# Performance work log

Measured on AMD Instinct MI355X. Metric: run time of the kernel, lower is better.

## Reference

```python
import jax, jax.numpy as jnp
import numpy as np

B, S, D, DFF, E, TOP_K = 4, 2048, 1024, 4096, 8, 2


def setup_inputs() -> dict:
    key = jax.random.key(0)
    ks = jax.random.split(key, 6)
    s = 0.02
    return {
        "x": jax.random.normal(ks[0], (B, S, D), dtype=jnp.float32),
        "gate_w": jax.random.normal(ks[1], (E, D), dtype=jnp.float32) * s,
        "w1": jax.random.normal(ks[2], (E, DFF, D), dtype=jnp.float32) * s,
        "b1": jax.random.normal(ks[3], (E, DFF), dtype=jnp.float32) * s,
        "w2": jax.random.normal(ks[4], (E, D, DFF), dtype=jnp.float32) * s,
        "b2": jax.random.normal(ks[5], (E, D), dtype=jnp.float32) * s,
    }


def _moe_forward(x, gate_w, w1, b1, w2, b2):
    b, s, d = x.shape
    xf = x.reshape(-1, d)                      # [T, D]
    T = xf.shape[0]
    e = gate_w.shape[0]
    logits = xf @ gate_w.T                     # [T, E]
    top_v, top_i = jax.lax.top_k(logits, TOP_K)  # [T, K]
    gw = jax.nn.softmax(top_v, axis=-1)          # [T, K]
    # load-balance loss (Switch Transformers): E * sum_i f_i * P_i
    probs = jax.nn.softmax(logits, axis=-1)
    f = jnp.mean(jax.nn.one_hot(jnp.argmax(logits, axis=-1), e, dtype=x.dtype), axis=0)
    lb_loss = e * jnp.sum(f * probs.mean(axis=0))
    # dense per-expert FFN (exact GELU, matching torch F.gelu default)
    h = jax.nn.gelu(jnp.einsum('td,efd->tef', xf, w1) + b1, approximate=False)  # [T,E,DFF]
    eo = jnp.einsum('tef,edf->ted', h, w2) + b2                                  # [T,E,D]
    # scatter top-k gate weights into dense [T, E] combine weights
    cw = jnp.zeros((T, e), dtype=x.dtype).at[jnp.arange(T)[:, None], top_i].add(gw)
    out = jnp.einsum('te,ted->td', cw, eo).reshape(b, s, d)
    return out, lb_loss


def reference(x, gate_w, w1, b1, w2, b2):
    return _moe_forward(x, gate_w, w1, b1, w2, b2)
```

## Files before the change

kernel.cpp:

```cpp
#include <hip/hip_runtime.h>
#include <cstdint>
#include <cstddef>

#define NEXP 8
#define NTOK 8192
#define DMODEL 1024
#define DFFN 4096
#define CAP 17408
#define MTILES (CAP / 128)

typedef __bf16 bf16;
typedef bf16 bf16x8 __attribute__((ext_vector_type(8)));
typedef float f32x4 __attribute__((ext_vector_type(4)));

static constexpr size_t OFF_HDR  = 0;
static constexpr size_t OFF_CNTH = 4096;
static constexpr size_t OFF_AMH  = OFF_CNTH + 65536;
static constexpr size_t OFF_PSH  = OFF_AMH + 65536;
static constexpr size_t OFF_TOKE = OFF_PSH + 65536;
static constexpr size_t OFF_TOKG = OFF_TOKE + 65536;
static constexpr size_t OFF_TOKS = OFF_TOKG + 65536;
static constexpr size_t OFF_BB   = OFF_TOKS + 65536;
static constexpr size_t OFF_XG   = OFF_BB + 65536;
static constexpr size_t OFF_W1B  = OFF_XG  + (size_t)CAP * DMODEL * 2;
static constexpr size_t OFF_W2B  = OFF_W1B + (size_t)NEXP * DFFN * DMODEL * 2;
static constexpr size_t OFF_H    = OFF_W2B + (size_t)NEXP * DMODEL * DFFN * 2;
static constexpr size_t OFF_O    = OFF_H   + (size_t)CAP * DFFN * 2;


__global__ void k_zero16(uint4* __restrict__ p) {
    p[(size_t)blockIdx.x * 256 + threadIdx.x] = make_uint4(0u, 0u, 0u, 0u);
}

__global__ void k_cvt(const float* __restrict__ s, bf16* __restrict__ d, int n8) {
    int i = blockIdx.x * 256 + threadIdx.x;
    if (i >= n8) return;
    const float4* sp = (const float4*)s;
    float4 a = sp[2 * i], b = sp[2 * i + 1];
    bf16x8 pk;
    pk[0] = (bf16)a.x; pk[1] = (bf16)a.y; pk[2] = (bf16)a.z; pk[3] = (bf16)a.w;
    pk[4] = (bf16)b.x; pk[5] = (bf16)b.y; pk[6] = (bf16)b.z; pk[7] = (bf16)b.w;
    ((bf16x8*)d)[i] = pk;
}

__global__ void k_gate(const float* __restrict__ x, const float* __restrict__ gwt,
                       int* __restrict__ cnth, int* __restrict__ amh, float* __restrict__ psh,
                       int* __restrict__ toke, float* __restrict__ tokg) {
    int tid = threadIdx.x, w = tid >> 6, lane = tid & 63;
    int t = blockIdx.x * 4 + w;
    __shared__ int s_cnt[8]; __shared__ int s_am[8]; __shared__ float s_ps[8];
    if (tid < 8) { s_cnt[tid] = 0; s_am[tid] = 0; s_ps[tid] = 0.f; }
    __syncthreads();
    float acc[8] = {0.f,0.f,0.f,0.f,0.f,0.f,0.f,0.f};
    const float4* xr = (const float4*)(x + (size_t)t * DMODEL);
#pragma unroll
    for (int c = 0; c < 4; c++) {
        float4 xv = xr[c * 64 + lane];
#pragma unroll
        for (int e = 0; e < 8; e++) {
            float4 wv = ((const float4*)(gwt + e * DMODEL))[c * 64 + lane];
            acc[e] = fmaf(xv.x, wv.x, fmaf(xv.y, wv.y, fmaf(xv.z, wv.z, fmaf(xv.w, wv.w, acc[e]))));
        }
    }
#pragma unroll
    for (int o = 32; o; o >>= 1) {
#pragma unroll
        for (int e = 0; e < 8; e++) acc[e] += __shfl_xor(acc[e], o);
    }
    if (lane == 0) {
        int i0 = 0; float v0 = acc[0];
#pragma unroll
        for (int e = 1; e < 8; e++) if (acc[e] > v0) { v0 = acc[e]; i0 = e; }
        int i1 = -1; float v1 = -1e30f;
#pragma unroll
        for (int e = 0; e < 8; e++) if (e != i0 && acc[e] > v1) { v1 = acc[e]; i1 = e; }
        float ex = expf(v1 - v0);
        float g0 = 1.f / (1.f + ex);
        float g1 = ex / (1.f + ex);
        toke[2 * t] = i0; toke[2 * t + 1] = i1;
        tokg[2 * t] = g0; tokg[2 * t + 1] = g1;
        atomicAdd(&s_cnt[i0], 1); atomicAdd(&s_cnt[i1], 1); atomicAdd(&s_am[i0], 1);
        float p[8], sum = 0.f;
#pragma unroll
        for (int e = 0; e < 8; e++) { p[e] = expf(acc[e] - v0); sum += p[e]; }
        float inv = 1.f / sum;
#pragma unroll
        for (int e = 0; e < 8; e++) atomicAdd(&s_ps[e], p[e] * inv);
    }
    __syncthreads();
    if (tid < 8) {
        cnth[blockIdx.x * 8 + tid] = s_cnt[tid];
        amh[blockIdx.x * 8 + tid]  = s_am[tid];
        psh[blockIdx.x * 8 + tid]  = s_ps[tid];
    }
}

__global__ void k_offsets(const int* __restrict__ cnth, const int* __restrict__ amh,
                          const float* __restrict__ psh, int* __restrict__ hdr,
                          int* __restrict__ bb, float* __restrict__ lb_out) {
    __shared__ int sc[8][256];
    __shared__ int sa[8][256];
    __shared__ float sp[8][256];
    __shared__ int sOff[8];
    int tid = threadIdx.x;
    int tc[8] = {0,0,0,0,0,0,0,0}, la[8] = {0,0,0,0,0,0,0,0};
    float lp[8] = {0.f,0.f,0.f,0.f,0.f,0.f,0.f,0.f};
    for (int j = 0; j < 8; j++) {
        int b = tid * 8 + j;
#pragma unroll
        for (int e = 0; e < 8; e++) { tc[e] += cnth[b * 8 + e]; la[e] += amh[b * 8 + e]; lp[e] += psh[b * 8 + e]; }
    }
#pragma unroll
    for (int e = 0; e < 8; e++) { sc[e][tid] = tc[e]; sa[e][tid] = la[e]; sp[e][tid] = lp[e]; }
    __syncthreads();
    for (int s = 1; s < 256; s <<= 1) {
        int add[8];
#pragma unroll
        for (int e = 0; e < 8; e++) add[e] = (tid >= s) ? sc[e][tid - s] : 0;
        __syncthreads();
#pragma unroll
        for (int e = 0; e < 8; e++) sc[e][tid] += add[e];
        __syncthreads();
    }
    for (int s = 128; s > 0; s >>= 1) {
        if (tid < s) {
#pragma unroll
            for (int e = 0; e < 8; e++) { sa[e][tid] += sa[e][tid + s]; sp[e][tid] += sp[e][tid + s]; }
        }
        __syncthreads();
    }
    if (tid == 0) {
        int run = 0; float lb = 0.f;
        for (int e = 0; e < 8; e++) {
            int c = sc[e][255];
            hdr[e] = c;
            hdr[16 + e] = run;
            int pad = ((c + 127) >> 7) << 7;
            hdr[24 + e] = pad;
            sOff[e] = run;
            run += pad;
            lb += ((float)sa[e][0] / (float)NTOK) * (sp[e][0] / (float)NTOK);
        }
        lb_out[0] = 8.f * lb;
    }
    __syncthreads();
    int excl[8];
#pragma unroll
    for (int e = 0; e < 8; e++) excl[e] = sOff[e] + sc[e][tid] - tc[e];
    for (int j = 0; j < 8; j++) {
        int b = tid * 8 + j;
#pragma unroll
        for (int e = 0; e < 8; e++) {
            bb[b * 8 + e] = excl[e];
            excl[e] += cnth[b * 8 + e];
        }
    }
}

__global__ void k_scatter(const float* __restrict__ x, const int* __restrict__ bb,
                          const int* __restrict__ toke, int* __restrict__ toks,
                          bf16* __restrict__ Xg) {
    int tid = threadIdx.x, w = tid >> 6, lane = tid & 63;
    int t = blockIdx.x * 4 + w;
    int a_e = (lane < 8) ? toke[blockIdx.x * 8 + lane] : 0;
    int e0 = __shfl(a_e, 2 * w), e1 = __shfl(a_e, 2 * w + 1);
    int r0 = 0, r1 = 0;
    for (int j = 0; j < 2 * w; j++) {
        int ej = __shfl(a_e, j);
        r0 += (ej == e0);
        r1 += (ej == e1);
    }
    int s0 = bb[blockIdx.x * 8 + e0] + r0;
    int s1 = bb[blockIdx.x * 8 + e1] + r1;
    if (lane == 0) { toks[2 * t] = s0; toks[2 * t + 1] = s1; }
    const float4* xr = (const float4*)(x + (size_t)t * DMODEL);
    bf16* d0 = Xg + (size_t)s0 * DMODEL;
    bf16* d1 = Xg + (size_t)s1 * DMODEL;
#pragma unroll
    for (int c = 0; c < 2; c++) {
        int base = c * 512 + lane * 8;
        float4 u = xr[base >> 2], v = xr[(base >> 2) + 1];
        bf16x8 pk;
        pk[0] = (bf16)u.x; pk[1] = (bf16)u.y; pk[2] = (bf16)u.z; pk[3] = (bf16)u.w;
        pk[4] = (bf16)v.x; pk[5] = (bf16)v.y; pk[6] = (bf16)v.z; pk[7] = (bf16)v.w;
        *(bf16x8*)(d0 + base) = pk;
        *(bf16x8*)(d1 + base) = pk;
    }
}

__device__ __forceinline__ void gll16(const bf16* g, bf16* l) {
    __builtin_amdgcn_global_load_lds((const __attribute__((address_space(1))) unsigned int*)g,
                                     (__attribute__((address_space(3))) unsigned int*)l, 16, 0, 0);
}

__device__ __forceinline__ float gelu_fast(float x) {
    float x3 = x * x * x;
    float z = fmaf(0.0713548163f, x3, 1.5957691216f * x);
    float s = __builtin_amdgcn_rcpf(1.0f + __expf(-z));
    return x * s;
}

template <int KD, int ND, bool GELU_BF16>
__global__ __launch_bounds__(256) void k_gemm(
    const bf16* __restrict__ Abase, const bf16* __restrict__ Wbase,
    const float* __restrict__ bias, void* __restrict__ Cbase,
    const int* __restrict__ hdr) {
    int flat = blockIdx.x;
    int g = flat % MTILES;
    int n = flat / MTILES;
    int row0 = g * 128;
    int total = hdr[16 + 7] + hdr[24 + 7];
    if (row0 >= total) return;
    int e = 0;
#pragma unroll
    for (int k = 1; k < 8; k++) e += (row0 >= hdr[16 + k]) ? 1 : 0;
    int nt = n * 128;

    const bf16* A = Abase + (size_t)row0 * KD;
    const bf16* W = Wbase + (size_t)e * ND * KD + (size_t)nt * KD;

    __shared__ bf16 As[128 * 64];
    __shared__ bf16 Bs[128 * 64];

    int tid = threadIdx.x, w = tid >> 6, lane = tid & 63;
    int lrow = lane >> 3;
    int lcolswz = ((lane & 7) ^ lrow) * 8;
    int wm = (w & 1) * 64, wn = (w >> 1) * 64;
    int fr = lane & 15, quad = lane >> 4;
    int swz = quad ^ (fr & 7);

    f32x4 acc[4][4] = {};

    for (int k0 = 0; k0 < KD; k0 += 64) {
#pragma unroll
        for (int i = 0; i < 4; i++) {
            int rb = w * 32 + i * 8;
            gll16(A + (size_t)(rb + lrow) * KD + k0 + lcolswz, &As[rb * 64]);
            gll16(W + (size_t)(rb + lrow) * KD + k0 + lcolswz, &Bs[rb * 64]);
        }
        __syncthreads();
#pragma unroll
        for (int kk = 0; kk < 64; kk += 32) {
            int coff = (swz ^ (kk >> 3)) * 8;
            bf16x8 af[4], bfr[4];
#pragma unroll
            for (int i = 0; i < 4; i++) af[i]  = *(const bf16x8*)&As[(wm + i * 16 + fr) * 64 + coff];
#pragma unroll
            for (int j = 0; j < 4; j++) bfr[j] = *(const bf16x8*)&Bs[(wn + j * 16 + fr) * 64 + coff];
#pragma unroll
            for (int i = 0; i < 4; i++)
#pragma unroll
                for (int j = 0; j < 4; j++)
                    acc[i][j] = __builtin_amdgcn_mfma_f32_16x16x32_bf16(af[i], bfr[j], acc[i][j], 0, 0, 0);
        }
        __syncthreads();
    }

#pragma unroll
    for (int j = 0; j < 4; j++) {
        int col = nt + wn + j * 16 + fr;
        float bv = bias[e * ND + col];
#pragma unroll
        for (int i = 0; i < 4; i++) {
#pragma unroll
            for (int r = 0; r < 4; r++) {
                int row = row0 + wm + i * 16 + quad * 4 + r;
                float v = acc[i][j][r] + bv;
                if (GELU_BF16) {
                    v = gelu_fast(v);
                    ((bf16*)Cbase)[(size_t)row * ND + col] = (bf16)v;
                } else {
                    ((float*)Cbase)[(size_t)row * ND + col] = v;
                }
            }
        }
    }
}

__global__ void k_combine(const float* __restrict__ O, const int* __restrict__ toks,
                          const float* __restrict__ tokg, float* __restrict__ out) {
    int t = blockIdx.x;
    int s0 = toks[2 * t], s1 = toks[2 * t + 1];
    float g0 = tokg[2 * t], g1 = tokg[2 * t + 1];
    const float4* o0 = (const float4*)(O + (size_t)s0 * DMODEL);
    const float4* o1 = (const float4*)(O + (size_t)s1 * DMODEL);
    float4* dst = (float4*)(out + (size_t)t * DMODEL);
    int i = threadIdx.x;
    float4 a = o0[i], b = o1[i];
    float4 r;
    r.x = g0 * a.x + g1 * b.x;
    r.y = g0 * a.y + g1 * b.y;
    r.z = g0 * a.z + g1 * b.z;
    r.w = g0 * a.w + g1 * b.w;
    dst[i] = r;
}

extern "C" void kernel_launch(void* const* d_in, const int* in_sizes, int n_in,
                              void* d_out, int out_size, void* d_ws, size_t ws_size,
                              hipStream_t stream) {
    const float* x   = (const float*)d_in[0];
    const float* gwt = (const float*)d_in[1];
    const float* w1  = (const float*)d_in[2];
    const float* b1  = (const float*)d_in[3];
    const float* w2  = (const float*)d_in[4];
    const float* b2  = (const float*)d_in[5];
    float* out = (float*)d_out;

    char* ws = (char*)d_ws;
    int*   hdr  = (int*)(ws + OFF_HDR);
    int*   cnth = (int*)(ws + OFF_CNTH);
    int*   amh  = (int*)(ws + OFF_AMH);
    float* psh  = (float*)(ws + OFF_PSH);
    int*   toke = (int*)(ws + OFF_TOKE);
    float* tokg = (float*)(ws + OFF_TOKG);
    int*   toks = (int*)(ws + OFF_TOKS);
    int*   bb   = (int*)(ws + OFF_BB);
    bf16*  Xg   = (bf16*)(ws + OFF_XG);
    bf16*  w1b  = (bf16*)(ws + OFF_W1B);
    bf16*  w2b  = (bf16*)(ws + OFF_W2B);
    bf16*  H    = (bf16*)(ws + OFF_H);
    float* O    = (float*)(ws + OFF_O);

    k_zero16<<<8704, 256, 0, stream>>>((uint4*)(ws + OFF_XG));
    k_cvt<<<16384, 256, 0, stream>>>(w1, w1b, 4194304);
    k_cvt<<<16384, 256, 0, stream>>>(w2, w2b, 4194304);
    k_gate<<<2048, 256, 0, stream>>>(x, gwt, cnth, amh, psh, toke, tokg);
    k_offsets<<<1, 256, 0, stream>>>(cnth, amh, psh, hdr, bb, out + (size_t)NTOK * DMODEL);
    k_scatter<<<2048, 256, 0, stream>>>(x, bb, toke, toks, Xg);
    k_gemm<DMODEL, DFFN, true><<<MTILES * (DFFN / 128), 256, 0, stream>>>(Xg, w1b, b1, (void*)H, hdr);
    k_gemm<DFFN, DMODEL, false><<<MTILES * (DMODEL / 128), 256, 0, stream>>>(H, w2b, b2, (void*)O, hdr);
    k_combine<<<NTOK, 256, 0, stream>>>(O, toks, tokg, out);
}
```

Before: 909.3 us.

## Pre-pack operands into MFMA fragment-major layout and drop LDS staging in GEMMs

Weights, gathered activations and the hidden tensor H are now stored in a fragment-major layout, where each 16-row by 32-k block is laid out exactly as the 16x16x32 MFMA expects. This lets the GEMM load operands straight from global memory into registers with double buffering, with no LDS tiles or block barriers in the main loop. Scatter is split into an index-only pass that builds an inverse map and a gather kernel that fills padding rows with zeros, so the separate zero-fill of Xg goes away. The trade-off is that blocks no longer share data through LDS, so global and L2 traffic rises. The first GEMM epilogue also needs an LDS transpose to write H in the packed layout.

New measurement: 1.050 ms. +15.5%, slower.

```diff
diff --git a/kernel.cpp b/kernel.cpp
--- a/kernel.cpp
+++ b/kernel.cpp
@@ -12,6 +12,7 @@
 typedef __bf16 bf16;
 typedef bf16 bf16x8 __attribute__((ext_vector_type(8)));
 typedef float f32x4 __attribute__((ext_vector_type(4)));
+
 
 static constexpr size_t OFF_HDR  = 0;
 static constexpr size_t OFF_CNTH = 4096;
@@ -21,26 +22,41 @@
 static constexpr size_t OFF_TOKG = OFF_TOKE + 65536;
 static constexpr size_t OFF_TOKS = OFF_TOKG + 65536;
 static constexpr size_t OFF_BB   = OFF_TOKS + 65536;
-static constexpr size_t OFF_XG   = OFF_BB + 65536;
+static constexpr size_t OFF_INV  = OFF_BB + 65536;
+static constexpr size_t OFF_XG   = OFF_INV + 73728;
 static constexpr size_t OFF_W1B  = OFF_XG  + (size_t)CAP * DMODEL * 2;
 static constexpr size_t OFF_W2B  = OFF_W1B + (size_t)NEXP * DFFN * DMODEL * 2;
 static constexpr size_t OFF_H    = OFF_W2B + (size_t)NEXP * DMODEL * DFFN * 2;
 static constexpr size_t OFF_O    = OFF_H   + (size_t)CAP * DFFN * 2;
 
 
-__global__ void k_zero16(uint4* __restrict__ p) {
-    p[(size_t)blockIdx.x * 256 + threadIdx.x] = make_uint4(0u, 0u, 0u, 0u);
-}
-
-__global__ void k_cvt(const float* __restrict__ s, bf16* __restrict__ d, int n8) {
-    int i = blockIdx.x * 256 + threadIdx.x;
-    if (i >= n8) return;
-    const float4* sp = (const float4*)s;
-    float4 a = sp[2 * i], b = sp[2 * i + 1];
-    bf16x8 pk;
-    pk[0] = (bf16)a.x; pk[1] = (bf16)a.y; pk[2] = (bf16)a.z; pk[3] = (bf16)a.w;
-    pk[4] = (bf16)b.x; pk[5] = (bf16)b.y; pk[6] = (bf16)b.z; pk[7] = (bf16)b.w;
-    ((bf16x8*)d)[i] = pk;
+__global__ void k_fillm1(int4* __restrict__ p) {
+    p[blockIdx.x * 256 + threadIdx.x] = make_int4(-1, -1, -1, -1);
+}
+
+template <int K>
+__global__ void k_cvt_fm(const float* __restrict__ w, bf16* __restrict__ wfm) {
+    constexpr int CB = K / 128;
+    __shared__ float ld[16][136];
+    int t = threadIdx.x;
+    int row = t >> 4, seg = t & 15;
+    int kbl = t >> 6, lane = t & 63, quad = lane >> 4, fr = lane & 15;
+    const float* src = w + (size_t)(blockIdx.x * 16 + row) * K + seg * 8;
+    bf16* dstg = wfm + (size_t)blockIdx.x * 16 * K + lane * 8;
+    for (int cb = 0; cb < CB; cb++) {
+        const float4* s = (const float4*)(src + cb * 128);
+        float4 u = s[0], v = s[1];
+        *(float4*)&ld[row][seg * 8] = u;
+        *(float4*)&ld[row][seg * 8 + 4] = v;
+        __syncthreads();
+        float4 a = *(const float4*)&ld[fr][kbl * 32 + quad * 8];
+        float4 b = *(const float4*)&ld[fr][kbl * 32 + quad * 8 + 4];
+        bf16x8 pk;
+        pk[0] = (bf16)a.x; pk[1] = (bf16)a.y; pk[2] = (bf16)a.z; pk[3] = (bf16)a.w;
+        pk[4] = (bf16)b.x; pk[5] = (bf16)b.y; pk[6] = (bf16)b.z; pk[7] = (bf16)b.w;
+        *(bf16x8*)(dstg + (size_t)(cb * 4 + kbl) * 512) = pk;
+        __syncthreads();
+    }
 }
 
 __global__ void k_gate(const float* __restrict__ x, const float* __restrict__ gwt,
@@ -157,40 +173,43 @@
     }
 }
 
-__global__ void k_scatter(const float* __restrict__ x, const int* __restrict__ bb,
-                          const int* __restrict__ toke, int* __restrict__ toks,
-                          bf16* __restrict__ Xg) {
+__global__ void k_scatter(const int* __restrict__ bb, const int* __restrict__ toke,
+                          int* __restrict__ toks, int* __restrict__ inv) {
+    int t = blockIdx.x * 256 + threadIdx.x;
+    int gb = t >> 2, k4 = t & 3;
+    int a[8];
+#pragma unroll
+    for (int j = 0; j < 8; j++) a[j] = toke[gb * 8 + j];
+    int e0 = a[2 * k4], e1 = a[2 * k4 + 1];
+    int r0 = 0, r1 = 0;
+    for (int j = 0; j < 2 * k4; j++) { r0 += (a[j] == e0); r1 += (a[j] == e1); }
+    int s0 = bb[gb * 8 + e0] + r0;
+    int s1 = bb[gb * 8 + e1] + r1;
+    toks[2 * t] = s0; toks[2 * t + 1] = s1;
+    inv[s0] = t; inv[s1] = t;
+}
+
+__global__ void k_gather(const float* __restrict__ x, const int* __restrict__ inv,
+                         bf16* __restrict__ Xg) {
+    int m16 = blockIdx.x;
     int tid = threadIdx.x, w = tid >> 6, lane = tid & 63;
-    int t = blockIdx.x * 4 + w;
-    int a_e = (lane < 8) ? toke[blockIdx.x * 8 + lane] : 0;
-    int e0 = __shfl(a_e, 2 * w), e1 = __shfl(a_e, 2 * w + 1);
-    int r0 = 0, r1 = 0;
-    for (int j = 0; j < 2 * w; j++) {
-        int ej = __shfl(a_e, j);
-        r0 += (ej == e0);
-        r1 += (ej == e1);
-    }
-    int s0 = bb[blockIdx.x * 8 + e0] + r0;
-    int s1 = bb[blockIdx.x * 8 + e1] + r1;
-    if (lane == 0) { toks[2 * t] = s0; toks[2 * t + 1] = s1; }
-    const float4* xr = (const float4*)(x + (size_t)t * DMODEL);
-    bf16* d0 = Xg + (size_t)s0 * DMODEL;
-    bf16* d1 = Xg + (size_t)s1 * DMODEL;
-#pragma unroll
-    for (int c = 0; c < 2; c++) {
-        int base = c * 512 + lane * 8;
-        float4 u = xr[base >> 2], v = xr[(base >> 2) + 1];
+    int quad = lane >> 4, fr = lane & 15;
+    int t16 = (lane < 16) ? inv[m16 * 16 + lane] : -1;
+    int tok = __shfl(t16, fr);
+    bf16* dst = Xg + (size_t)m16 * 32 * 512 + lane * 8;
+    for (int kb = w * 8; kb < w * 8 + 8; kb++) {
         bf16x8 pk;
-        pk[0] = (bf16)u.x; pk[1] = (bf16)u.y; pk[2] = (bf16)u.z; pk[3] = (bf16)u.w;
-        pk[4] = (bf16)v.x; pk[5] = (bf16)v.y; pk[6] = (bf16)v.z; pk[7] = (bf16)v.w;
-        *(bf16x8*)(d0 + base) = pk;
-        *(bf16x8*)(d1 + base) = pk;
-    }
-}
-
-__device__ __forceinline__ void gll16(const bf16* g, bf16* l) {
-    __builtin_amdgcn_global_load_lds((const __attribute__((address_space(1))) unsigned int*)g,
-                                     (__attribute__((address_space(3))) unsigned int*)l, 16, 0, 0);
+        if (tok >= 0) {
+            const float4* s = (const float4*)(x + (size_t)tok * DMODEL + kb * 32 + quad * 8);
+            float4 u = s[0], v = s[1];
+            pk[0] = (bf16)u.x; pk[1] = (bf16)u.y; pk[2] = (bf16)u.z; pk[3] = (bf16)u.w;
+            pk[4] = (bf16)v.x; pk[5] = (bf16)v.y; pk[6] = (bf16)v.z; pk[7] = (bf16)v.w;
+        } else {
+#pragma unroll
+            for (int j = 0; j < 8; j++) pk[j] = (bf16)0.f;
+        }
+        *(bf16x8*)(dst + (size_t)kb * 512) = pk;
+    }
 }
 
 __device__ __forceinline__ float gelu_fast(float x) {
@@ -202,9 +221,10 @@
 
 template <int KD, int ND, bool GELU_BF16>
 __global__ __launch_bounds__(256) void k_gemm(
-    const bf16* __restrict__ Abase, const bf16* __restrict__ Wbase,
+    const bf16* __restrict__ Afm, const bf16* __restrict__ Wfm,
     const float* __restrict__ bias, void* __restrict__ Cbase,
     const int* __restrict__ hdr) {
+    constexpr int KB = KD / 32;
     int flat = blockIdx.x;
     int g = flat % MTILES;
     int n = flat / MTILES;
@@ -216,61 +236,89 @@
     for (int k = 1; k < 8; k++) e += (row0 >= hdr[16 + k]) ? 1 : 0;
     int nt = n * 128;
 
-    const bf16* A = Abase + (size_t)row0 * KD;
-    const bf16* W = Wbase + (size_t)e * ND * KD + (size_t)nt * KD;
-
-    __shared__ bf16 As[128 * 64];
-    __shared__ bf16 Bs[128 * 64];
-
     int tid = threadIdx.x, w = tid >> 6, lane = tid & 63;
-    int lrow = lane >> 3;
-    int lcolswz = ((lane & 7) ^ lrow) * 8;
     int wm = (w & 1) * 64, wn = (w >> 1) * 64;
     int fr = lane & 15, quad = lane >> 4;
-    int swz = quad ^ (fr & 7);
+
+    const bf16* pA[4];
+    const bf16* pB[4];
+#pragma unroll
+    for (int i = 0; i < 4; i++) {
+        int m16 = ((row0 + wm) >> 4) + i;
+        pA[i] = Afm + (size_t)m16 * KB * 512 + lane * 8;
+        int n16 = ((nt + wn) >> 4) + i;
+        pB[i] = Wfm + (size_t)e * ND * KD + (size_t)n16 * KB * 512 + lane * 8;
+    }
 
     f32x4 acc[4][4] = {};
-
-    for (int k0 = 0; k0 < KD; k0 += 64) {
+    bf16x8 a0[4], b0[4], a1[4], b1[4];
+#pragma unroll
+    for (int i = 0; i < 4; i++) { a0[i] = *(const bf16x8*)(pA[i]); b0[i] = *(const bf16x8*)(pB[i]); }
+
+    for (int kb = 0; kb < KB; kb += 2) {
 #pragma unroll
         for (int i = 0; i < 4; i++) {
-            int rb = w * 32 + i * 8;
-            gll16(A + (size_t)(rb + lrow) * KD + k0 + lcolswz, &As[rb * 64]);
-            gll16(W + (size_t)(rb + lrow) * KD + k0 + lcolswz, &Bs[rb * 64]);
-        }
-        __syncthreads();
-#pragma unroll
-        for (int kk = 0; kk < 64; kk += 32) {
-            int coff = (swz ^ (kk >> 3)) * 8;
-            bf16x8 af[4], bfr[4];
-#pragma unroll
-            for (int i = 0; i < 4; i++) af[i]  = *(const bf16x8*)&As[(wm + i * 16 + fr) * 64 + coff];
-#pragma unroll
-            for (int j = 0; j < 4; j++) bfr[j] = *(const bf16x8*)&Bs[(wn + j * 16 + fr) * 64 + coff];
-#pragma unroll
-            for (int i = 0; i < 4; i++)
-#pragma unroll
-                for (int j = 0; j < 4; j++)
-                    acc[i][j] = __builtin_amdgcn_mfma_f32_16x16x32_bf16(af[i], bfr[j], acc[i][j], 0, 0, 0);
-        }
-        __syncthreads();
-    }
-
-#pragma unroll
-    for (int j = 0; j < 4; j++) {
-        int col = nt + wn + j * 16 + fr;
-        float bv = bias[e * ND + col];
-#pragma unroll
-        for (int i = 0; i < 4; i++) {
-#pragma unroll
-            for (int r = 0; r < 4; r++) {
-                int row = row0 + wm + i * 16 + quad * 4 + r;
-                float v = acc[i][j][r] + bv;
-                if (GELU_BF16) {
-                    v = gelu_fast(v);
-                    ((bf16*)Cbase)[(size_t)row * ND + col] = (bf16)v;
-                } else {
-                    ((float*)Cbase)[(size_t)row * ND + col] = v;
+            a1[i] = *(const bf16x8*)(pA[i] + (size_t)(kb + 1) * 512);
+            b1[i] = *(const bf16x8*)(pB[i] + (size_t)(kb + 1) * 512);
+        }
+#pragma unroll
+        for (int i = 0; i < 4; i++)
+#pragma unroll
+            for (int j = 0; j < 4; j++)
+                acc[i][j] = __builtin_amdgcn_mfma_f32_16x16x32_bf16(a0[i], b0[j], acc[i][j], 0, 0, 0);
+        if (kb + 2 < KB) {
+#pragma unroll
+            for (int i = 0; i < 4; i++) {
+                a0[i] = *(const bf16x8*)(pA[i] + (size_t)(kb + 2) * 512);
+                b0[i] = *(const bf16x8*)(pB[i] + (size_t)(kb + 2) * 512);
+            }
+        }
+#pragma unroll
+        for (int i = 0; i < 4; i++)
+#pragma unroll
+            for (int j = 0; j < 4; j++)
+                acc[i][j] = __builtin_amdgcn_mfma_f32_16x16x32_bf16(a1[i], b1[j], acc[i][j], 0, 0, 0);
+    }
+
+    if constexpr (GELU_BF16) {
+        __shared__ bf16 Ct[128 * 136];
+#pragma unroll
+        for (int j = 0; j < 4; j++) {
+            int lc = wn + j * 16 + fr;
+            float bv = bias[e * ND + nt + lc];
+#pragma unroll
+            for (int i = 0; i < 4; i++) {
+#pragma unroll
+                for (int r = 0; r < 4; r++) {
+                    int lr = wm + i * 16 + quad * 4 + r;
+                    Ct[lr * 136 + lc] = (bf16)gelu_fast(acc[i][j][r] + bv);
+                }
+            }
+        }
+        __syncthreads();
+        bf16* Hfm = (bf16*)Cbase;
+        constexpr int KBH = ND / 32;
+#pragma unroll
+        for (int li = 0; li < 8; li++) {
+            int line = w * 8 + li;
+            int mg = line >> 2, kbl = line & 3;
+            bf16x8 v = *(const bf16x8*)&Ct[(mg * 16 + fr) * 136 + kbl * 32 + quad * 8];
+            size_t m16 = (size_t)(row0 >> 4) + mg;
+            size_t kbG = (size_t)(nt >> 5) + kbl;
+            *(bf16x8*)(Hfm + (m16 * KBH + kbG) * 512 + lane * 8) = v;
+        }
+    } else {
+        float* Ob = (float*)Cbase;
+#pragma unroll
+        for (int j = 0; j < 4; j++) {
+            int col = nt + wn + j * 16 + fr;
+            float bv = bias[e * ND + col];
+#pragma unroll
+            for (int i = 0; i < 4; i++) {
+#pragma unroll
+                for (int r = 0; r < 4; r++) {
+                    int row = row0 + wm + i * 16 + quad * 4 + r;
+                    Ob[(size_t)row * ND + col] = acc[i][j][r] + bv;
                 }
             }
         }
@@ -315,18 +363,20 @@
     float* tokg = (float*)(ws + OFF_TOKG);
     int*   toks = (int*)(ws + OFF_TOKS);
     int*   bb   = (int*)(ws + OFF_BB);
+    int*   inv  = (int*)(ws + OFF_INV);
     bf16*  Xg   = (bf16*)(ws + OFF_XG);
     bf16*  w1b  = (bf16*)(ws + OFF_W1B);
     bf16*  w2b  = (bf16*)(ws + OFF_W2B);
     bf16*  H    = (bf16*)(ws + OFF_H);
     float* O    = (float*)(ws + OFF_O);
 
-    k_zero16<<<8704, 256, 0, stream>>>((uint4*)(ws + OFF_XG));
-    k_cvt<<<16384, 256, 0, stream>>>(w1, w1b, 4194304);
-    k_cvt<<<16384, 256, 0, stream>>>(w2, w2b, 4194304);
+    k_fillm1<<<17, 256, 0, stream>>>((int4*)inv);
+    k_cvt_fm<DMODEL><<<NEXP * DFFN / 16, 256, 0, stream>>>(w1, w1b);
+    k_cvt_fm<DFFN><<<NEXP * DMODEL / 16, 256, 0, stream>>>(w2, w2b);
     k_gate<<<2048, 256, 0, stream>>>(x, gwt, cnth, amh, psh, toke, tokg);
     k_offsets<<<1, 256, 0, stream>>>(cnth, amh, psh, hdr, bb, out + (size_t)NTOK * DMODEL);
-    k_scatter<<<2048, 256, 0, stream>>>(x, bb, toke, toks, Xg);
+    k_scatter<<<32, 256, 0, stream>>>(bb, toke, toks, inv);
+    k_gather<<<CAP / 16, 256, 0, stream>>>(x, inv, Xg);
     k_gemm<DMODEL, DFFN, true><<<MTILES * (DFFN / 128), 256, 0, stream>>>(Xg, w1b, b1, (void*)H, hdr);
     k_gemm<DFFN, DMODEL, false><<<MTILES * (DMODEL / 128), 256, 0, stream>>>(H, w2b, b2, (void*)O, hdr);
     k_combine<<<NTOK, 256, 0, stream>>>(O, toks, tokg, out);
```

## Fuse gated combine into second GEMM epilogue via atomic scatter-add

Applied to the files above, without the earlier changes.

Removes the fp32 intermediate O buffer and the separate combine kernel. The second expert GEMM now multiplies each row by its gate weight and atomically adds it into the token's output row, using an inverse slot-to-token map built during scatter. A new init kernel zeroes the output, and padding slots are marked -1 so they are skipped. The GEMM block index is also remapped to interleave M tiles across n tiles, which changes the order tiles are scheduled. In exchange it pays for fp32 atomics on the output and makes the summation order nondeterministic.

Result: slower. 968.0 us (+6.5%).

```diff
diff --git a/kernel.cpp b/kernel.cpp
--- a/kernel.cpp
+++ b/kernel.cpp
@@ -15,21 +15,28 @@
 
 static constexpr size_t OFF_HDR  = 0;
 static constexpr size_t OFF_CNTH = 4096;
-static constexpr size_t OFF_AMH  = OFF_CNTH + 65536;
-static constexpr size_t OFF_PSH  = OFF_AMH + 65536;
-static constexpr size_t OFF_TOKE = OFF_PSH + 65536;
-static constexpr size_t OFF_TOKG = OFF_TOKE + 65536;
-static constexpr size_t OFF_TOKS = OFF_TOKG + 65536;
-static constexpr size_t OFF_BB   = OFF_TOKS + 65536;
-static constexpr size_t OFF_XG   = OFF_BB + 65536;
+static constexpr size_t OFF_AMH  = 69632;
+static constexpr size_t OFF_PSH  = 135168;
+static constexpr size_t OFF_TOKE = 200704;
+static constexpr size_t OFF_TOKG = 266240;
+static constexpr size_t OFF_BB   = 331776;
+static constexpr size_t OFF_GWS  = 397312;
+static constexpr size_t OFF_INV  = 471040;
+static constexpr size_t OFF_XG   = 544768;
 static constexpr size_t OFF_W1B  = OFF_XG  + (size_t)CAP * DMODEL * 2;
 static constexpr size_t OFF_W2B  = OFF_W1B + (size_t)NEXP * DFFN * DMODEL * 2;
 static constexpr size_t OFF_H    = OFF_W2B + (size_t)NEXP * DMODEL * DFFN * 2;
-static constexpr size_t OFF_O    = OFF_H   + (size_t)CAP * DFFN * 2;
-
-
-__global__ void k_zero16(uint4* __restrict__ p) {
-    p[(size_t)blockIdx.x * 256 + threadIdx.x] = make_uint4(0u, 0u, 0u, 0u);
+
+__global__ void k_init(float4* __restrict__ outz, uint4* __restrict__ xg,
+                       int4* __restrict__ inv) {
+    int b = blockIdx.x, t = threadIdx.x;
+    if (b < 8192) {
+        outz[(size_t)b * 256 + t] = make_float4(0.f, 0.f, 0.f, 0.f);
+    } else if (b < 8192 + 8704) {
+        xg[(size_t)(b - 8192) * 256 + t] = make_uint4(0u, 0u, 0u, 0u);
+    } else {
+        inv[(size_t)(b - 16896) * 256 + t] = make_int4(-1, -1, -1, -1);
+    }
 }
 
 __global__ void k_cvt(const float* __restrict__ s, bf16* __restrict__ d, int n8) {
@@ -158,7 +165,8 @@
 }
 
 __global__ void k_scatter(const float* __restrict__ x, const int* __restrict__ bb,
-                          const int* __restrict__ toke, int* __restrict__ toks,
+                          const int* __restrict__ toke, const float* __restrict__ tokg,
+                          int* __restrict__ inv, float* __restrict__ gws,
                           bf16* __restrict__ Xg) {
     int tid = threadIdx.x, w = tid >> 6, lane = tid & 63;
     int t = blockIdx.x * 4 + w;
@@ -172,7 +180,10 @@
     }
     int s0 = bb[blockIdx.x * 8 + e0] + r0;
     int s1 = bb[blockIdx.x * 8 + e1] + r1;
-    if (lane == 0) { toks[2 * t] = s0; toks[2 * t + 1] = s1; }
+    if (lane == 0) {
+        inv[s0] = t; inv[s1] = t;
+        gws[s0] = tokg[2 * t]; gws[s1] = tokg[2 * t + 1];
+    }
     const float4* xr = (const float4*)(x + (size_t)t * DMODEL);
     bf16* d0 = Xg + (size_t)s0 * DMODEL;
     bf16* d1 = Xg + (size_t)s1 * DMODEL;
@@ -204,10 +215,12 @@
 __global__ __launch_bounds__(256) void k_gemm(
     const bf16* __restrict__ Abase, const bf16* __restrict__ Wbase,
     const float* __restrict__ bias, void* __restrict__ Cbase,
-    const int* __restrict__ hdr) {
+    const int* __restrict__ hdr, const int* __restrict__ inv,
+    const float* __restrict__ gws) {
     int flat = blockIdx.x;
-    int g = flat % MTILES;
-    int n = flat / MTILES;
+    int rest = flat >> 3;
+    int g = (flat & 7) * 17 + (rest % 17);
+    int n = rest / 17;
     int row0 = g * 128;
     int total = hdr[16 + 7] + hdr[24 + 7];
     if (row0 >= total) return;
@@ -221,6 +234,8 @@
 
     __shared__ bf16 As[128 * 64];
     __shared__ bf16 Bs[128 * 64];
+    __shared__ int s_inv[128];
+    __shared__ float s_gw[128];
 
     int tid = threadIdx.x, w = tid >> 6, lane = tid & 63;
     int lrow = lane >> 3;
@@ -256,43 +271,40 @@
         __syncthreads();
     }
 
-#pragma unroll
-    for (int j = 0; j < 4; j++) {
-        int col = nt + wn + j * 16 + fr;
-        float bv = bias[e * ND + col];
-#pragma unroll
-        for (int i = 0; i < 4; i++) {
-#pragma unroll
-            for (int r = 0; r < 4; r++) {
-                int row = row0 + wm + i * 16 + quad * 4 + r;
-                float v = acc[i][j][r] + bv;
-                if (GELU_BF16) {
-                    v = gelu_fast(v);
-                    ((bf16*)Cbase)[(size_t)row * ND + col] = (bf16)v;
-                } else {
-                    ((float*)Cbase)[(size_t)row * ND + col] = v;
+    if constexpr (GELU_BF16) {
+#pragma unroll
+        for (int j = 0; j < 4; j++) {
+            int col = nt + wn + j * 16 + fr;
+            float bv = bias[e * ND + col];
+#pragma unroll
+            for (int i = 0; i < 4; i++) {
+#pragma unroll
+                for (int r = 0; r < 4; r++) {
+                    int row = row0 + wm + i * 16 + quad * 4 + r;
+                    ((bf16*)Cbase)[(size_t)row * ND + col] = (bf16)gelu_fast(acc[i][j][r] + bv);
                 }
             }
         }
-    }
-}
-
-__global__ void k_combine(const float* __restrict__ O, const int* __restrict__ toks,
-                          const float* __restrict__ tokg, float* __restrict__ out) {
-    int t = blockIdx.x;
-    int s0 = toks[2 * t], s1 = toks[2 * t + 1];
-    float g0 = tokg[2 * t], g1 = tokg[2 * t + 1];
-    const float4* o0 = (const float4*)(O + (size_t)s0 * DMODEL);
-    const float4* o1 = (const float4*)(O + (size_t)s1 * DMODEL);
-    float4* dst = (float4*)(out + (size_t)t * DMODEL);
-    int i = threadIdx.x;
-    float4 a = o0[i], b = o1[i];
-    float4 r;
-    r.x = g0 * a.x + g1 * b.x;
-    r.y = g0 * a.y + g1 * b.y;
-    r.z = g0 * a.z + g1 * b.z;
-    r.w = g0 * a.w + g1 * b.w;
-    dst[i] = r;
+    } else {
+        if (tid < 128) { s_inv[tid] = inv[row0 + tid]; s_gw[tid] = gws[row0 + tid]; }
+        __syncthreads();
+        float* outp = (float*)Cbase;
+#pragma unroll
+        for (int j = 0; j < 4; j++) {
+            int col = nt + wn + j * 16 + fr;
+            float bv = bias[e * ND + col];
+#pragma unroll
+            for (int i = 0; i < 4; i++) {
+#pragma unroll
+                for (int r = 0; r < 4; r++) {
+                    int lr = wm + i * 16 + quad * 4 + r;
+                    int tok = s_inv[lr];
+                    if (tok >= 0)
+                        atomicAdd(outp + (size_t)tok * ND + col, s_gw[lr] * (acc[i][j][r] + bv));
+                }
+            }
+        }
+    }
 }
 
 extern "C" void kernel_launch(void* const* d_in, const int* in_sizes, int n_in,
@@ -313,21 +325,22 @@
     float* psh  = (float*)(ws + OFF_PSH);
     int*   toke = (int*)(ws + OFF_TOKE);
     float* tokg = (float*)(ws + OFF_TOKG);
-    int*   toks = (int*)(ws + OFF_TOKS);
     int*   bb   = (int*)(ws + OFF_BB);
+    float* gws  = (float*)(ws + OFF_GWS);
+    int*   inv  = (int*)(ws + OFF_INV);
     bf16*  Xg   = (bf16*)(ws + OFF_XG);
     bf16*  w1b  = (bf16*)(ws + OFF_W1B);
     bf16*  w2b  = (bf16*)(ws + OFF_W2B);
     bf16*  H    = (bf16*)(ws + OFF_H);
-    float* O    = (float*)(ws + OFF_O);
-
-    k_zero16<<<8704, 256, 0, stream>>>((uint4*)(ws + OFF_XG));
+
+    k_init<<<16913, 256, 0, stream>>>((float4*)out, (uint4*)Xg, (int4*)inv);
     k_cvt<<<16384, 256, 0, stream>>>(w1, w1b, 4194304);
     k_cvt<<<16384, 256, 0, stream>>>(w2, w2b, 4194304);
     k_gate<<<2048, 256, 0, stream>>>(x, gwt, cnth, amh, psh, toke, tokg);
     k_offsets<<<1, 256, 0, stream>>>(cnth, amh, psh, hdr, bb, out + (size_t)NTOK * DMODEL);
-    k_scatter<<<2048, 256, 0, stream>>>(x, bb, toke, toks, Xg);
-    k_gemm<DMODEL, DFFN, true><<<MTILES * (DFFN / 128), 256, 0, stream>>>(Xg, w1b, b1, (void*)H, hdr);
-    k_gemm<DFFN, DMODEL, false><<<MTILES * (DMODEL / 128), 256, 0, stream>>>(H, w2b, b2, (void*)O, hdr);
-    k_combine<<<NTOK, 256, 0, stream>>>(O, toks, tokg, out);
-}
+    k_scatter<<<2048, 256, 0, stream>>>(x, bb, toke, tokg, inv, gws, Xg);
+    k_gemm<DMODEL, DFFN, true><<<MTILES * (DFFN / 128), 256, 0, stream>>>(
+        Xg, w1b, b1, (void*)H, hdr, nullptr, nullptr);
+    k_gemm<DFFN, DMODEL, false><<<MTILES * (DMODEL / 128), 256, 0, stream>>>(
+        H, w2b, b2, (void*)out, hdr, inv, gws);
+}
```
